# Performance work log

Hardware: AMD Instinct MI355X
Metric: run time of the kernel (lower is better)

The kernel has to match this reference:

```python
import jax, jax.numpy as jnp
import numpy as np

DIM = 4096
N_HEADS = 32
N_KV_HEADS = 8
HEAD_DIM = 128
EPS = 1e-6
B, S = 1, 2048


def setup_inputs() -> dict:
    key = jax.random.key(0)
    ks = jax.random.split(key, 8)
    x = jax.random.normal(ks[0], (B, S, DIM), dtype=jnp.float32)
    # Standard RoPE cos/sin table, broadcast to (B, S, HEAD_DIM)
    inv_freq = 1.0 / (10000.0 ** (np.arange(0, HEAD_DIM, 2, dtype=np.float32) / HEAD_DIM))
    t = np.arange(S, dtype=np.float32)
    freqs = np.outer(t, inv_freq)  # (S, HEAD_DIM/2)
    emb = np.concatenate([freqs, freqs], axis=-1)  # (S, HEAD_DIM)
    cos = jnp.broadcast_to(jnp.cos(emb)[None], (B, S, HEAD_DIM))
    sin = jnp.broadcast_to(jnp.sin(emb)[None], (B, S, HEAD_DIM))
    std = 0.02
    wq = jax.random.normal(ks[1], (N_HEADS * HEAD_DIM, DIM), dtype=jnp.float32) * std
    wk = jax.random.normal(ks[2], (N_KV_HEADS * HEAD_DIM, DIM), dtype=jnp.float32) * std
    wv = jax.random.normal(ks[3], (N_KV_HEADS * HEAD_DIM, DIM), dtype=jnp.float32) * std
    wo = jax.random.normal(ks[4], (DIM, N_HEADS * HEAD_DIM), dtype=jnp.float32) * std
    q_norm_w = jnp.ones((HEAD_DIM,), dtype=jnp.float32) + 0.1 * jax.random.normal(ks[5], (HEAD_DIM,), dtype=jnp.float32)
    k_norm_w = jnp.ones((HEAD_DIM,), dtype=jnp.float32) + 0.1 * jax.random.normal(ks[6], (HEAD_DIM,), dtype=jnp.float32)
    return {"x": x, "cos": cos, "sin": sin, "wq": wq, "wk": wk, "wv": wv,
            "wo": wo, "q_norm_w": q_norm_w, "k_norm_w": k_norm_w}


def _rmsnorm(x, w):
    var = jnp.mean(jnp.square(x), axis=-1, keepdims=True)
    return x * jax.lax.rsqrt(var + EPS) * w


def _rotate_half(x):
    h = x.shape[-1] // 2
    return jnp.concatenate([-x[..., h:], x[..., :h]], axis=-1)


def reference(x, cos, sin, wq, wk, wv, wo, q_norm_w, k_norm_w):
    bs, seqlen, _ = x.shape
    # QKV projections (Linear with weight of shape (out, in), no bias)
    xq = (x @ wq.T).reshape(bs, seqlen, N_HEADS, HEAD_DIM)
    xk = (x @ wk.T).reshape(bs, seqlen, N_KV_HEADS, HEAD_DIM)
    xv = (x @ wv.T).reshape(bs, seqlen, N_KV_HEADS, HEAD_DIM)
    # QK RMSNorm (after projection, before RoPE)
    xq = _rmsnorm(xq, q_norm_w)
    xk = _rmsnorm(xk, k_norm_w)
    # RoPE: cos/sin (B, S, D) -> broadcast over head axis
    c = cos[:, :, None, :]
    s = sin[:, :, None, :]
    xq = xq * c + _rotate_half(xq) * s
    xk = xk * c + _rotate_half(xk) * s
    # GQA: repeat kv heads
    n_rep = N_HEADS // N_KV_HEADS
    xk = jnp.repeat(xk, n_rep, axis=2)
    xv = jnp.repeat(xv, n_rep, axis=2)
    # (B, H, S, D)
    q = xq.transpose(0, 2, 1, 3)
    k = xk.transpose(0, 2, 1, 3)
    v = xv.transpose(0, 2, 1, 3)
    scale = HEAD_DIM ** -0.5
    scores = jnp.einsum('bhqd,bhkd->bhqk', q, k) * scale
    causal = jnp.tril(jnp.ones((seqlen, seqlen), dtype=bool))
    scores = jnp.where(causal, scores, jnp.finfo(scores.dtype).min)
    probs = jax.nn.softmax(scores, axis=-1)
    out = jnp.einsum('bhqk,bhkd->bhqd', probs, v)
    out = out.transpose(0, 2, 1, 3).reshape(bs, seqlen, N_HEADS * HEAD_DIM)
    return out @ wo.T
```

## Files before the change

kernel.cpp:

```cpp
#include <hip/hip_runtime.h>


#define S_LEN 2048
#define DIM 4096
#define NH 32
#define NKV 8
#define HD 128
#define SCALE 0.08838834764831845f

typedef __attribute__((ext_vector_type(8))) short short8;
typedef __attribute__((ext_vector_type(4))) float f32x4;

__device__ __forceinline__ float bf2f(unsigned short u) {
  union { unsigned i; float f; } c; c.i = ((unsigned)u) << 16; return c.f;
}
__device__ __forceinline__ unsigned short f2bf(float f) {
  union { float f; unsigned u; } c; c.f = f;
  return (unsigned short)((c.u + 0x7fffu + ((c.u >> 16) & 1u)) >> 16);
}
__device__ __forceinline__ void cvt8(const float* __restrict__ g,
                                     unsigned short* __restrict__ d) {
  const float4 a = *(const float4*)g;
  const float4 b = *(const float4*)(g + 4);
  short8 p;
  p[0] = (short)f2bf(a.x); p[1] = (short)f2bf(a.y);
  p[2] = (short)f2bf(a.z); p[3] = (short)f2bf(a.w);
  p[4] = (short)f2bf(b.x); p[5] = (short)f2bf(b.y);
  p[6] = (short)f2bf(b.z); p[7] = (short)f2bf(b.w);
  *(short8*)d = p;
}
__device__ __forceinline__ void storeC(float* p, float v) { *p = v; }
__device__ __forceinline__ void storeC(unsigned short* p, float v) { *p = f2bf(v); }

#define G_X   1048576u
#define G_WQ  2097152u
#define G_WK   524288u
#define G_WV   524288u
#define G_QKV (G_WQ + G_WK + G_WV)

__global__ __launch_bounds__(256)
void cvt_all(const float* __restrict__ x,  const float* __restrict__ wq,
             const float* __restrict__ wk, const float* __restrict__ wv,
             const float* __restrict__ wo,
             unsigned short* __restrict__ xb,
             unsigned short* __restrict__ wqkvb,
             unsigned short* __restrict__ wob) {
  const size_t g = (size_t)blockIdx.x * 256 + threadIdx.x;
  if (g < G_X) {
    cvt8(x + g * 8, xb + g * 8);
  } else if (g < G_X + G_QKV) {
    const size_t o = g - G_X;
    const float* s = (o < G_WQ) ? wq + o * 8
                   : (o < G_WQ + G_WK) ? wk + (o - G_WQ) * 8
                                       : wv + (o - G_WQ - G_WK) * 8;
    cvt8(s, wqkvb + o * 8);
  } else {
    const size_t o = g - (G_X + G_QKV);
    cvt8(wo + o * 8, wob + o * 8);
  }
}

template <int QKV, typename TC>
__global__ __launch_bounds__(256)
void gemm16(const unsigned short* __restrict__ A,
            const unsigned short* __restrict__ B,
            TC* __restrict__ C0,
            unsigned short* __restrict__ Ck,
            unsigned short* __restrict__ Cv, int K) {
  __shared__ unsigned short lsA[128 * 64];
  __shared__ unsigned short lsB[128 * 64];

  const int t    = threadIdx.x;
  const int lane = t & 63;
  const int w    = t >> 6;
  const int m0   = blockIdx.y * 128;
  const int n0   = blockIdx.x * 128;

  f32x4 acc[4][4];
#pragma unroll
  for (int a = 0; a < 4; ++a)
#pragma unroll
    for (int b = 0; b < 4; ++b)
#pragma unroll
      for (int e = 0; e < 4; ++e) acc[a][b][e] = 0.f;

  const int l15  = lane & 15;
  const int qd   = lane >> 4;
  const int wr   = w >> 1, wc = w & 1;
  const int sr8  = lane >> 3;
  const int skg  = (lane & 7) ^ sr8;
  const int l7   = l15 & 7;

  const int nkb = K >> 6;
  for (int kb = 0; kb < nkb; ++kb) {
    const int k0 = kb << 6;
#pragma unroll
    for (int c = 0; c < 4; ++c) {
      const int chunk = c * 4 + w;
      const int row   = chunk * 8 + sr8;
      const unsigned short* ga = A + (size_t)(m0 + row) * K + k0 + skg * 8;
      const unsigned short* gb = B + (size_t)(n0 + row) * K + k0 + skg * 8;
      __builtin_amdgcn_global_load_lds(
          (const __attribute__((address_space(1))) void*)ga,
          (__attribute__((address_space(3))) void*)(lsA + chunk * 512), 16, 0, 0);
      __builtin_amdgcn_global_load_lds(
          (const __attribute__((address_space(1))) void*)gb,
          (__attribute__((address_space(3))) void*)(lsB + chunk * 512), 16, 0, 0);
    }
    asm volatile("s_waitcnt vmcnt(0)" ::: "memory");
    __syncthreads();

#pragma unroll
    for (int half = 0; half < 2; ++half) {
      const int kg = (half * 4 + qd) ^ l7;
      short8 af[4], bf[4];
#pragma unroll
      for (int mi = 0; mi < 4; ++mi)
        af[mi] = *(const short8*)(lsA + (wr * 64 + mi * 16 + l15) * 64 + kg * 8);
#pragma unroll
      for (int ni = 0; ni < 4; ++ni)
        bf[ni] = *(const short8*)(lsB + (wc * 64 + ni * 16 + l15) * 64 + kg * 8);
#pragma unroll
      for (int mi = 0; mi < 4; ++mi)
#pragma unroll
        for (int ni = 0; ni < 4; ++ni)
          acc[mi][ni] = __builtin_amdgcn_mfma_f32_16x16x32_bf16(
              af[mi], bf[ni], acc[mi][ni], 0, 0, 0);
    }
    __syncthreads();
  }

#pragma unroll
  for (int mi = 0; mi < 4; ++mi)
#pragma unroll
    for (int i = 0; i < 4; ++i) {
      const int grow = m0 + wr * 64 + mi * 16 + qd * 4 + i;
#pragma unroll
      for (int ni = 0; ni < 4; ++ni) {
        const int gcol = n0 + wc * 64 + ni * 16 + l15;
        if (QKV) {
          if (n0 < 4096)
            storeC((unsigned short*)C0 + (size_t)grow * 4096 + gcol,
                   acc[mi][ni][i]);
          else if (n0 < 5120)
            Ck[(size_t)grow * 1024 + (gcol - 4096)] = f2bf(acc[mi][ni][i]);
          else
            Cv[(size_t)(gcol - 5120) * S_LEN + grow] = f2bf(acc[mi][ni][i]);
        } else {
          storeC(C0 + (size_t)grow * 4096 + gcol, acc[mi][ni][i]);
        }
      }
    }
}

__global__ __launch_bounds__(128)
void norm_rope(unsigned short* __restrict__ qb, unsigned short* __restrict__ kb,
               const float* __restrict__ cosb, const float* __restrict__ sinb,
               const float* __restrict__ qw, const float* __restrict__ kw) {
  const int hIdx = blockIdx.x;
  const int s    = blockIdx.y;
  const int d    = threadIdx.x;

  unsigned short* p; const float* wt;
  if (hIdx < NH) { p = qb + (size_t)s * (NH * HD) + hIdx * HD + d; wt = qw; }
  else           { p = kb + (size_t)s * (NKV * HD) + (hIdx - NH) * HD + d; wt = kw; }

  const float v = bf2f(*p);
  float ss = v * v;
  for (int off = 32; off; off >>= 1) ss += __shfl_down(ss, off);
  __shared__ float red[2];
  __shared__ float xs[128];
  if ((d & 63) == 0) red[d >> 6] = ss;
  __syncthreads();
  const float tot = red[0] + red[1];
  const float r   = rsqrtf(tot * (1.f / 128.f) + 1e-6f);
  const float xn  = v * r * wt[d];
  xs[d] = xn;
  __syncthreads();
  const float rot = (d < 64) ? -xs[d + 64] : xs[d - 64];
  float o = xn * cosb[s * HD + d] + rot * sinb[s * HD + d];
  if (hIdx < NH) o *= SCALE;
  *p = f2bf(o);
}

#define PSTR 72

__global__ __launch_bounds__(256)
void attn_mfma(const unsigned short* __restrict__ qB,
               const unsigned short* __restrict__ kB,
               const unsigned short* __restrict__ vT,
               unsigned short* __restrict__ oB) {
  __shared__ unsigned short ks[64 * 128];
  __shared__ unsigned short vt[128 * 64];
  __shared__ unsigned short Ps[4 * 16 * PSTR];

  const int t    = threadIdx.x;
  const int lane = t & 63;
  const int w    = t >> 6;
  const int qt   = (gridDim.x - 1) - blockIdx.x;
  const int h    = blockIdx.y;
  const int kvh  = h >> 2;
  const int l15  = lane & 15;
  const int qd   = lane >> 4;
  const int l7   = l15 & 7;

  const int kr16 = lane >> 4;
  const int vr8  = lane >> 3;
  const int vkg  = (lane & 7) ^ (vr8 & 7);

  short8 qf[4];
  {
    const unsigned short* qp =
        qB + (size_t)(qt * 64 + w * 16 + l15) * (NH * HD) + h * HD + qd * 8;
#pragma unroll
    for (int s = 0; s < 4; ++s) qf[s] = *(const short8*)(qp + s * 32);
  }

  f32x4 O[8];
#pragma unroll
  for (int nt = 0; nt < 8; ++nt)
#pragma unroll
    for (int e = 0; e < 4; ++e) O[nt][e] = 0.f;
  float l_i[4] = {0.f, 0.f, 0.f, 0.f};

  unsigned short* Pw = Ps + w * (16 * PSTR);

  for (int kt = 0; kt <= qt; ++kt) {
#pragma unroll
    for (int c = 0; c < 4; ++c) {
      const int chunk = w * 4 + c;
      const int key = chunk * 4 + kr16;
      const int dg  = (lane & 15) ^ (key & 15);
      const unsigned short* gk = kB + (size_t)(kt * 64 + key) * (NKV * HD) +
                                 kvh * HD + dg * 8;
      __builtin_amdgcn_global_load_lds(
          (const __attribute__((address_space(1))) void*)gk,
          (__attribute__((address_space(3))) void*)(ks + chunk * 512), 16, 0, 0);
      const int dv = chunk * 8 + vr8;
      const unsigned short* gv = vT + (size_t)(kvh * HD + dv) * S_LEN +
                                 kt * 64 + vkg * 8;
      __builtin_amdgcn_global_load_lds(
          (const __attribute__((address_space(1))) void*)gv,
          (__attribute__((address_space(3))) void*)(vt + chunk * 512), 16, 0, 0);
    }
    asm volatile("s_waitcnt vmcnt(0)" ::: "memory");
    __syncthreads();

    f32x4 S[4];
#pragma unroll
    for (int ct = 0; ct < 4; ++ct) {
#pragma unroll
      for (int e = 0; e < 4; ++e) S[ct][e] = 0.f;
#pragma unroll
      for (int s = 0; s < 4; ++s) {
        const int kg = (s * 4 + qd) ^ l15;
        const short8 kf =
            *(const short8*)(ks + (ct * 16 + l15) * 128 + kg * 8);
        S[ct] = __builtin_amdgcn_mfma_f32_16x16x32_bf16(qf[s], kf, S[ct], 0, 0, 0);
      }
    }

    if (kt == qt) {
#pragma unroll
      for (int ct = 0; ct < 4; ++ct)
#pragma unroll
        for (int i = 0; i < 4; ++i) {
          const int rloc = w * 16 + qd * 4 + i;
          const int cloc = ct * 16 + l15;
          if (cloc > rloc) S[ct][i] = -1e30f;
        }
    }

#pragma unroll
    for (int ct = 0; ct < 4; ++ct)
#pragma unroll
      for (int i = 0; i < 4; ++i) {
        const float e = __expf(S[ct][i]);
        l_i[i] += e;
        Pw[(qd * 4 + i) * PSTR + ct * 16 + l15] = f2bf(e);
      }

    {
      const short8 pf0 = *(const short8*)(Pw + l15 * PSTR + qd * 8);
      const short8 pf1 = *(const short8*)(Pw + l15 * PSTR + 32 + qd * 8);
#pragma unroll
      for (int nt = 0; nt < 8; ++nt) {
        const int kg0 = qd ^ l7;
        const int kg1 = (4 + qd) ^ l7;
        const short8 vf0 =
            *(const short8*)(vt + (nt * 16 + l15) * 64 + kg0 * 8);
        O[nt] = __builtin_amdgcn_mfma_f32_16x16x32_bf16(pf0, vf0, O[nt], 0, 0, 0);
        const short8 vf1 =
            *(const short8*)(vt + (nt * 16 + l15) * 64 + kg1 * 8);
        O[nt] = __builtin_amdgcn_mfma_f32_16x16x32_bf16(pf1, vf1, O[nt], 0, 0, 0);
      }
    }
    __syncthreads();
  }

  float linv[4];
#pragma unroll
  for (int i = 0; i < 4; ++i) {
    float s = l_i[i];
#pragma unroll
    for (int off = 1; off < 16; off <<= 1) s += __shfl_xor(s, off);
    linv[i] = 1.f / s;
  }
#pragma unroll
  for (int nt = 0; nt < 8; ++nt)
#pragma unroll
    for (int i = 0; i < 4; ++i) {
      const size_t row = (size_t)(qt * 64 + w * 16 + qd * 4 + i);
      oB[row * (NH * HD) + h * HD + nt * 16 + l15] = f2bf(O[nt][i] * linv[i]);
    }
}

extern "C" void kernel_launch(void* const* d_in, const int* in_sizes, int n_in,
                              void* d_out, int out_size, void* d_ws, size_t ws_size,
                              hipStream_t stream) {
  const float* x    = (const float*)d_in[0];
  const float* cosb = (const float*)d_in[1];
  const float* sinb = (const float*)d_in[2];
  const float* wq   = (const float*)d_in[3];
  const float* wk   = (const float*)d_in[4];
  const float* wv   = (const float*)d_in[5];
  const float* wo   = (const float*)d_in[6];
  const float* qnw  = (const float*)d_in[7];
  const float* knw  = (const float*)d_in[8];

  unsigned short* q     = (unsigned short*)d_ws;
  unsigned short* k     = q + (size_t)S_LEN * DIM;
  unsigned short* vT    = k + (size_t)S_LEN * NKV * HD;
  unsigned short* att   = vT + (size_t)NKV * HD * S_LEN;
  unsigned short* xb    = att + (size_t)S_LEN * DIM;
  unsigned short* wqkvb = xb + (size_t)S_LEN * DIM;
  unsigned short* wob   = wqkvb + (size_t)6144 * DIM;

  cvt_all<<<dim3(24576), dim3(256), 0, stream>>>(x, wq, wk, wv, wo, xb, wqkvb,
                                                 wob);
  gemm16<1, unsigned short>
      <<<dim3(48, 16), dim3(256), 0, stream>>>(xb, wqkvb, q, k, vT, DIM);
  norm_rope<<<dim3(NH + NKV, S_LEN), dim3(128), 0, stream>>>(q, k, cosb, sinb,
                                                             qnw, knw);
  attn_mfma<<<dim3(S_LEN / 64, NH), dim3(256), 0, stream>>>(q, k, vT, att);
  gemm16<0, float>
      <<<dim3(32, 16), dim3(256), 0, stream>>>(att, wob, (float*)d_out,
                                               nullptr, nullptr, DIM);
}
```

Baseline: 572.9 us.

## Replace 128x128 GEMM with 256x256 double-buffered pipelined GEMM using 8 waves

Replaces the single-buffered 128x128 tile GEMM with a 256x256 tile kernel of 512 threads. Half-tiles of A and B are staged into a 128KB double-buffered LDS region while MFMAs run on the other half, with barriers and s_setprio around the math. The aim is to hide global-load latency and raise data reuse per byte loaded. The catch is that the grid shrinks to 192 and 128 blocks, which is below one block per CU on a 256-CU part, and each block has one-block-per-CU LDS occupancy.

```diff
diff --git a/kernel.cpp b/kernel.cpp
--- a/kernel.cpp
+++ b/kernel.cpp
@@ -7,6 +7,7 @@
 #define NKV 8
 #define HD 128
 #define SCALE 0.08838834764831845f
+#define NKT 64
 
 typedef __attribute__((ext_vector_type(8))) short short8;
 typedef __attribute__((ext_vector_type(4))) float f32x4;
@@ -60,94 +61,144 @@
   }
 }
 
+
+#define STAGE(XB, G0, HH, KT, LOFF)                                           \
+  {                                                                            \
+    _Pragma("unroll")                                                          \
+    for (int j = 0; j < 2; ++j) {                                              \
+      const int chunk = (w << 1) + j;                                          \
+      const unsigned short* ga = (XB) +                                        \
+          (size_t)((G0) + (HH) * 128 + chunk * 8 + r8) * 4096 +                \
+          ((KT) << 6) + gsw;                                                   \
+      __builtin_amdgcn_global_load_lds(                                        \
+          (const __attribute__((address_space(1))) void*)ga,                   \
+          (__attribute__((address_space(3))) void*)(ls + (LOFF) +              \
+                                                    (HH) * 8192 + chunk * 512),\
+          16, 0, 0);                                                           \
+    }                                                                          \
+  }
+
+#define LDA(mq)                                                                \
+  _Pragma("unroll") for (int mi = 0; mi < 4; ++mi)                             \
+  _Pragma("unroll") for (int kc = 0; kc < 2; ++kc)                             \
+    af[mi][kc] = *(const short8*)(ls + aoff +                                  \
+        ((mq) * 128 + wr * 64 + mi * 16 + l15) * 64 +                          \
+        (((kc << 2) + qd) ^ l7) * 8);
+
+#define LDB(nq)                                                                \
+  _Pragma("unroll") for (int ni = 0; ni < 2; ++ni)                             \
+  _Pragma("unroll") for (int kc = 0; kc < 2; ++kc)                             \
+    bfr[nq][ni][kc] = *(const short8*)(ls + boff +                             \
+        ((nq) * 128 + wc * 32 + ni * 16 + l15) * 64 +                          \
+        (((kc << 2) + qd) ^ l7) * 8);
+
+#define MM(mq, nq)                                                             \
+  __builtin_amdgcn_s_setprio(1);                                               \
+  _Pragma("unroll") for (int mi = 0; mi < 4; ++mi)                             \
+  _Pragma("unroll") for (int ni = 0; ni < 2; ++ni)                             \
+  _Pragma("unroll") for (int kc = 0; kc < 2; ++kc)                             \
+    acc[(mq) * 4 + mi][(nq) * 2 + ni] =                                        \
+        __builtin_amdgcn_mfma_f32_16x16x32_bf16(                               \
+            af[mi][kc], bfr[nq][ni][kc], acc[(mq) * 4 + mi][(nq) * 2 + ni],    \
+            0, 0, 0);                                                          \
+  __builtin_amdgcn_s_setprio(0);
+
 template <int QKV, typename TC>
-__global__ __launch_bounds__(256)
-void gemm16(const unsigned short* __restrict__ A,
-            const unsigned short* __restrict__ B,
-            TC* __restrict__ C0,
-            unsigned short* __restrict__ Ck,
-            unsigned short* __restrict__ Cv, int K) {
-  __shared__ unsigned short lsA[128 * 64];
-  __shared__ unsigned short lsB[128 * 64];
+__global__ __launch_bounds__(512)
+void gemm256(const unsigned short* __restrict__ A,
+             const unsigned short* __restrict__ B,
+             TC* __restrict__ C0,
+             unsigned short* __restrict__ Ck,
+             unsigned short* __restrict__ Cv) {
+  __shared__ unsigned short ls[65536];
 
   const int t    = threadIdx.x;
   const int lane = t & 63;
   const int w    = t >> 6;
-  const int m0   = blockIdx.y * 128;
-  const int n0   = blockIdx.x * 128;
-
-  f32x4 acc[4][4];
-#pragma unroll
-  for (int a = 0; a < 4; ++a)
-#pragma unroll
-    for (int b = 0; b < 4; ++b)
-#pragma unroll
-      for (int e = 0; e < 4; ++e) acc[a][b][e] = 0.f;
-
+  const int wr   = w >> 2;
+  const int wc   = w & 3;
+  const int m0   = blockIdx.y * 256;
+  const int n0   = blockIdx.x * 256;
   const int l15  = lane & 15;
   const int qd   = lane >> 4;
-  const int wr   = w >> 1, wc = w & 1;
-  const int sr8  = lane >> 3;
-  const int skg  = (lane & 7) ^ sr8;
   const int l7   = l15 & 7;
-
-  const int nkb = K >> 6;
-  for (int kb = 0; kb < nkb; ++kb) {
-    const int k0 = kb << 6;
-#pragma unroll
-    for (int c = 0; c < 4; ++c) {
-      const int chunk = c * 4 + w;
-      const int row   = chunk * 8 + sr8;
-      const unsigned short* ga = A + (size_t)(m0 + row) * K + k0 + skg * 8;
-      const unsigned short* gb = B + (size_t)(n0 + row) * K + k0 + skg * 8;
-      __builtin_amdgcn_global_load_lds(
-          (const __attribute__((address_space(1))) void*)ga,
-          (__attribute__((address_space(3))) void*)(lsA + chunk * 512), 16, 0, 0);
-      __builtin_amdgcn_global_load_lds(
-          (const __attribute__((address_space(1))) void*)gb,
-          (__attribute__((address_space(3))) void*)(lsB + chunk * 512), 16, 0, 0);
-    }
-    asm volatile("s_waitcnt vmcnt(0)" ::: "memory");
-    __syncthreads();
-
-#pragma unroll
-    for (int half = 0; half < 2; ++half) {
-      const int kg = (half * 4 + qd) ^ l7;
-      short8 af[4], bf[4];
-#pragma unroll
-      for (int mi = 0; mi < 4; ++mi)
-        af[mi] = *(const short8*)(lsA + (wr * 64 + mi * 16 + l15) * 64 + kg * 8);
-#pragma unroll
-      for (int ni = 0; ni < 4; ++ni)
-        bf[ni] = *(const short8*)(lsB + (wc * 64 + ni * 16 + l15) * 64 + kg * 8);
-#pragma unroll
-      for (int mi = 0; mi < 4; ++mi)
-#pragma unroll
-        for (int ni = 0; ni < 4; ++ni)
-          acc[mi][ni] = __builtin_amdgcn_mfma_f32_16x16x32_bf16(
-              af[mi], bf[ni], acc[mi][ni], 0, 0, 0);
-    }
-    __syncthreads();
-  }
-
-#pragma unroll
-  for (int mi = 0; mi < 4; ++mi)
+  const int r8   = lane >> 3;
+  const int gsw  = ((lane & 7) ^ r8) * 8;
+
+  f32x4 acc[8][4];
+#pragma unroll
+  for (int a = 0; a < 8; ++a)
+#pragma unroll
+    for (int b = 0; b < 4; ++b)
+#pragma unroll
+      for (int e = 0; e < 4; ++e) acc[a][b][e] = 0.f;
+
+  short8 af[4][2];
+  short8 bfr[2][2][2];
+
+  STAGE(A, m0, 0, 0, 0);
+  STAGE(B, n0, 1, 0, 16384);
+  STAGE(A, m0, 1, 0, 0);
+  STAGE(B, n0, 0, 0, 16384);
+  STAGE(A, m0, 0, 1, 32768);
+  STAGE(B, n0, 1, 1, 49152);
+  asm volatile("s_waitcnt vmcnt(4)" ::: "memory");
+  __builtin_amdgcn_s_barrier();
+
+#pragma unroll 2
+  for (int kt = 0; kt < NKT; ++kt) {
+    const int p    = kt & 1;
+    const int base = p << 15;
+    const int ob   = base ^ 32768;
+    const int aoff = base;
+    const int boff = base + 16384;
+    const int kn1  = (kt + 1 < NKT) ? kt + 1 : NKT - 1;
+    const int kn2  = (kt + 2 < NKT) ? kt + 2 : NKT - 1;
+
+    LDA(0);
+    LDB(0);
+    STAGE(A, m0, 1, kn1, ob);
+    __builtin_amdgcn_s_barrier();
+    MM(0, 0);
+    __builtin_amdgcn_s_barrier();
+
+    LDB(1);
+    STAGE(B, n0, 0, kn1, ob + 16384);
+    __builtin_amdgcn_s_barrier();
+    MM(0, 1);
+    __builtin_amdgcn_s_barrier();
+
+    LDA(1);
+    STAGE(A, m0, 0, kn2, base);
+    __builtin_amdgcn_s_barrier();
+    MM(1, 1);
+    __builtin_amdgcn_s_barrier();
+
+    STAGE(B, n0, 1, kn2, base + 16384);
+    __builtin_amdgcn_s_barrier();
+    MM(1, 0);
+    asm volatile("s_waitcnt vmcnt(4)" ::: "memory");
+    __builtin_amdgcn_s_barrier();
+  }
+
+#pragma unroll
+  for (int fm = 0; fm < 8; ++fm)
 #pragma unroll
     for (int i = 0; i < 4; ++i) {
-      const int grow = m0 + wr * 64 + mi * 16 + qd * 4 + i;
-#pragma unroll
-      for (int ni = 0; ni < 4; ++ni) {
-        const int gcol = n0 + wc * 64 + ni * 16 + l15;
+      const int grow = m0 + (fm >> 2) * 128 + wr * 64 + (fm & 3) * 16 + qd * 4 + i;
+#pragma unroll
+      for (int fn = 0; fn < 4; ++fn) {
+        const int gcol = n0 + (fn >> 1) * 128 + wc * 32 + (fn & 1) * 16 + l15;
+        const float v  = acc[fm][fn][i];
         if (QKV) {
           if (n0 < 4096)
-            storeC((unsigned short*)C0 + (size_t)grow * 4096 + gcol,
-                   acc[mi][ni][i]);
+            storeC((unsigned short*)C0 + (size_t)grow * 4096 + gcol, v);
           else if (n0 < 5120)
-            Ck[(size_t)grow * 1024 + (gcol - 4096)] = f2bf(acc[mi][ni][i]);
+            Ck[(size_t)grow * 1024 + (gcol - 4096)] = f2bf(v);
           else
-            Cv[(size_t)(gcol - 5120) * S_LEN + grow] = f2bf(acc[mi][ni][i]);
+            Cv[(size_t)(gcol - 5120) * S_LEN + grow] = f2bf(v);
         } else {
-          storeC(C0 + (size_t)grow * 4096 + gcol, acc[mi][ni][i]);
+          storeC(C0 + (size_t)grow * 4096 + gcol, v);
         }
       }
     }
@@ -338,12 +389,12 @@
 
   cvt_all<<<dim3(24576), dim3(256), 0, stream>>>(x, wq, wk, wv, wo, xb, wqkvb,
                                                  wob);
-  gemm16<1, unsigned short>
-      <<<dim3(48, 16), dim3(256), 0, stream>>>(xb, wqkvb, q, k, vT, DIM);
+  gemm256<1, unsigned short>
+      <<<dim3(24, 8), dim3(512), 0, stream>>>(xb, wqkvb, q, k, vT);
   norm_rope<<<dim3(NH + NKV, S_LEN), dim3(128), 0, stream>>>(q, k, cosb, sinb,
                                                              qnw, knw);
   attn_mfma<<<dim3(S_LEN / 64, NH), dim3(256), 0, stream>>>(q, k, vT, att);
-  gemm16<0, float>
-      <<<dim3(32, 16), dim3(256), 0, stream>>>(att, wob, (float*)d_out,
-                                               nullptr, nullptr, DIM);
-}
+  gemm256<0, float>
+      <<<dim3(16, 8), dim3(512), 0, stream>>>(att, wob, (float*)d_out,
+                                              nullptr, nullptr);
+}
```

New measurement: 589.7 us. +2.9%, slower.

## Double attention query tile to 128 rows per block and streamline norm_rope

Applied to the files above, without the earlier changes.

The attention kernel now handles 128 query rows per block, with each wave owning two 16-row fragments. Each K/V tile loaded into LDS is therefore reused by twice as many MFMAs, which halves K/V global traffic per query. On the diagonal tile, waves whose rows are fully masked skip their work, and query tiles are ordered in reverse for half the heads to balance load across blocks. norm_rope is rewritten so one wave handles a whole head, using wave shuffles with no LDS or barriers, and each block processes 8 heads. The cost is higher register pressure from doubled accumulators and fewer, larger attention blocks (16x32 grid).

```diff
diff --git a/kernel.cpp b/kernel.cpp
--- a/kernel.cpp
+++ b/kernel.cpp
@@ -153,34 +153,35 @@
     }
 }
 
-__global__ __launch_bounds__(128)
+__global__ __launch_bounds__(512)
 void norm_rope(unsigned short* __restrict__ qb, unsigned short* __restrict__ kb,
                const float* __restrict__ cosb, const float* __restrict__ sinb,
                const float* __restrict__ qw, const float* __restrict__ kw) {
-  const int hIdx = blockIdx.x;
-  const int s    = blockIdx.y;
-  const int d    = threadIdx.x;
+  const int s    = blockIdx.x;
+  const int w    = threadIdx.x >> 6;
+  const int l    = threadIdx.x & 63;
+  const int hh   = blockIdx.y * 8 + w;
 
   unsigned short* p; const float* wt;
-  if (hIdx < NH) { p = qb + (size_t)s * (NH * HD) + hIdx * HD + d; wt = qw; }
-  else           { p = kb + (size_t)s * (NKV * HD) + (hIdx - NH) * HD + d; wt = kw; }
-
-  const float v = bf2f(*p);
-  float ss = v * v;
-  for (int off = 32; off; off >>= 1) ss += __shfl_down(ss, off);
-  __shared__ float red[2];
-  __shared__ float xs[128];
-  if ((d & 63) == 0) red[d >> 6] = ss;
-  __syncthreads();
-  const float tot = red[0] + red[1];
-  const float r   = rsqrtf(tot * (1.f / 128.f) + 1e-6f);
-  const float xn  = v * r * wt[d];
-  xs[d] = xn;
-  __syncthreads();
-  const float rot = (d < 64) ? -xs[d + 64] : xs[d - 64];
-  float o = xn * cosb[s * HD + d] + rot * sinb[s * HD + d];
-  if (hIdx < NH) o *= SCALE;
-  *p = f2bf(o);
+  if (hh < NH) { p = qb + (size_t)s * (NH * HD) + hh * HD; wt = qw; }
+  else         { p = kb + (size_t)s * (NKV * HD) + (hh - NH) * HD; wt = kw; }
+
+  const float v0 = bf2f(p[l]);
+  const float v1 = bf2f(p[l + 64]);
+  float ss = v0 * v0 + v1 * v1;
+#pragma unroll
+  for (int off = 32; off; off >>= 1) ss += __shfl_xor(ss, off);
+  const float r = rsqrtf(ss * (1.f / 128.f) + 1e-6f);
+
+  const float xn0 = v0 * r * wt[l];
+  const float xn1 = v1 * r * wt[l + 64];
+  const float c0 = cosb[s * HD + l],      s0 = sinb[s * HD + l];
+  const float c1 = cosb[s * HD + l + 64], s1 = sinb[s * HD + l + 64];
+  float o0 = xn0 * c0 - xn1 * s0;
+  float o1 = xn1 * c1 + xn0 * s1;
+  if (hh < NH) { o0 *= SCALE; o1 *= SCALE; }
+  p[l]      = f2bf(o0);
+  p[l + 64] = f2bf(o1);
 }
 
 #define PSTR 72
@@ -192,13 +193,14 @@
                unsigned short* __restrict__ oB) {
   __shared__ unsigned short ks[64 * 128];
   __shared__ unsigned short vt[128 * 64];
-  __shared__ unsigned short Ps[4 * 16 * PSTR];
+  __shared__ unsigned short Ps[4 * 32 * PSTR];
 
   const int t    = threadIdx.x;
   const int lane = t & 63;
   const int w    = t >> 6;
-  const int qt   = (gridDim.x - 1) - blockIdx.x;
   const int h    = blockIdx.y;
+  const int qt   = (h & 16) ? (15 - blockIdx.x) : blockIdx.x;
+  const int q0   = qt * 128;
   const int kvh  = h >> 2;
   const int l15  = lane & 15;
   const int qd   = lane >> 4;
@@ -208,24 +210,28 @@
   const int vr8  = lane >> 3;
   const int vkg  = (lane & 7) ^ (vr8 & 7);
 
-  short8 qf[4];
-  {
+  short8 qf[2][4];
+#pragma unroll
+  for (int f = 0; f < 2; ++f) {
     const unsigned short* qp =
-        qB + (size_t)(qt * 64 + w * 16 + l15) * (NH * HD) + h * HD + qd * 8;
-#pragma unroll
-    for (int s = 0; s < 4; ++s) qf[s] = *(const short8*)(qp + s * 32);
+        qB + (size_t)(q0 + w * 32 + f * 16 + l15) * (NH * HD) + h * HD + qd * 8;
+#pragma unroll
+    for (int s = 0; s < 4; ++s) qf[f][s] = *(const short8*)(qp + s * 32);
   }
 
-  f32x4 O[8];
-#pragma unroll
-  for (int nt = 0; nt < 8; ++nt)
-#pragma unroll
-    for (int e = 0; e < 4; ++e) O[nt][e] = 0.f;
-  float l_i[4] = {0.f, 0.f, 0.f, 0.f};
-
-  unsigned short* Pw = Ps + w * (16 * PSTR);
-
-  for (int kt = 0; kt <= qt; ++kt) {
+  f32x4 O[2][8];
+#pragma unroll
+  for (int f = 0; f < 2; ++f)
+#pragma unroll
+    for (int nt = 0; nt < 8; ++nt)
+#pragma unroll
+      for (int e = 0; e < 4; ++e) O[f][nt][e] = 0.f;
+  float l_i[2][4] = {{0.f, 0.f, 0.f, 0.f}, {0.f, 0.f, 0.f, 0.f}};
+
+  unsigned short* Pw = Ps + w * (32 * PSTR);
+
+  const int nkt = 2 * qt + 2;
+  for (int kt = 0; kt < nkt; ++kt) {
 #pragma unroll
     for (int c = 0; c < 4; ++c) {
       const int chunk = w * 4 + c;
@@ -246,73 +252,99 @@
     asm volatile("s_waitcnt vmcnt(0)" ::: "memory");
     __syncthreads();
 
-    f32x4 S[4];
-#pragma unroll
-    for (int ct = 0; ct < 4; ++ct) {
-#pragma unroll
-      for (int e = 0; e < 4; ++e) S[ct][e] = 0.f;
-#pragma unroll
-      for (int s = 0; s < 4; ++s) {
-        const int kg = (s * 4 + qd) ^ l15;
-        const short8 kf =
-            *(const short8*)(ks + (ct * 16 + l15) * 128 + kg * 8);
-        S[ct] = __builtin_amdgcn_mfma_f32_16x16x32_bf16(qf[s], kf, S[ct], 0, 0, 0);
-      }
-    }
-
-    if (kt == qt) {
-#pragma unroll
-      for (int ct = 0; ct < 4; ++ct)
-#pragma unroll
-        for (int i = 0; i < 4; ++i) {
-          const int rloc = w * 16 + qd * 4 + i;
-          const int cloc = ct * 16 + l15;
-          if (cloc > rloc) S[ct][i] = -1e30f;
+    const int dk = kt - 2 * qt;
+    const bool active = (dk <= 0) || (w >= 2);
+    if (active) {
+      f32x4 S[2][4];
+#pragma unroll
+      for (int ct = 0; ct < 4; ++ct) {
+#pragma unroll
+        for (int e = 0; e < 4; ++e) { S[0][ct][e] = 0.f; S[1][ct][e] = 0.f; }
+#pragma unroll
+        for (int s = 0; s < 4; ++s) {
+          const int kg = (s * 4 + qd) ^ l15;
+          const short8 kf =
+              *(const short8*)(ks + (ct * 16 + l15) * 128 + kg * 8);
+          S[0][ct] = __builtin_amdgcn_mfma_f32_16x16x32_bf16(qf[0][s], kf,
+                                                             S[0][ct], 0, 0, 0);
+          S[1][ct] = __builtin_amdgcn_mfma_f32_16x16x32_bf16(qf[1][s], kf,
+                                                             S[1][ct], 0, 0, 0);
         }
-    }
-
-#pragma unroll
-    for (int ct = 0; ct < 4; ++ct)
-#pragma unroll
-      for (int i = 0; i < 4; ++i) {
-        const float e = __expf(S[ct][i]);
-        l_i[i] += e;
-        Pw[(qd * 4 + i) * PSTR + ct * 16 + l15] = f2bf(e);
-      }
-
-    {
-      const short8 pf0 = *(const short8*)(Pw + l15 * PSTR + qd * 8);
-      const short8 pf1 = *(const short8*)(Pw + l15 * PSTR + 32 + qd * 8);
-#pragma unroll
-      for (int nt = 0; nt < 8; ++nt) {
+      }
+
+      if (dk >= 0) {
+#pragma unroll
+        for (int f = 0; f < 2; ++f)
+#pragma unroll
+          for (int ct = 0; ct < 4; ++ct)
+#pragma unroll
+            for (int i = 0; i < 4; ++i) {
+              const int krel = dk * 64 + ct * 16 + l15;
+              const int rrel = w * 32 + f * 16 + qd * 4 + i;
+              if (krel > rrel) S[f][ct][i] = -1e30f;
+            }
+      }
+
+#pragma unroll
+      for (int f = 0; f < 2; ++f)
+#pragma unroll
+        for (int ct = 0; ct < 4; ++ct)
+#pragma unroll
+          for (int i = 0; i < 4; ++i) {
+            const float e = __expf(S[f][ct][i]);
+            l_i[f][i] += e;
+            Pw[(f * 16 + qd * 4 + i) * PSTR + ct * 16 + l15] = f2bf(e);
+          }
+
+      {
+        short8 pf[2][2];
+#pragma unroll
+        for (int f = 0; f < 2; ++f) {
+          pf[f][0] = *(const short8*)(Pw + (f * 16 + l15) * PSTR + qd * 8);
+          pf[f][1] = *(const short8*)(Pw + (f * 16 + l15) * PSTR + 32 + qd * 8);
+        }
         const int kg0 = qd ^ l7;
         const int kg1 = (4 + qd) ^ l7;
-        const short8 vf0 =
-            *(const short8*)(vt + (nt * 16 + l15) * 64 + kg0 * 8);
-        O[nt] = __builtin_amdgcn_mfma_f32_16x16x32_bf16(pf0, vf0, O[nt], 0, 0, 0);
-        const short8 vf1 =
-            *(const short8*)(vt + (nt * 16 + l15) * 64 + kg1 * 8);
-        O[nt] = __builtin_amdgcn_mfma_f32_16x16x32_bf16(pf1, vf1, O[nt], 0, 0, 0);
+#pragma unroll
+        for (int nt = 0; nt < 8; ++nt) {
+          const short8 vf0 =
+              *(const short8*)(vt + (nt * 16 + l15) * 64 + kg0 * 8);
+          const short8 vf1 =
+              *(const short8*)(vt + (nt * 16 + l15) * 64 + kg1 * 8);
+          O[0][nt] = __builtin_amdgcn_mfma_f32_16x16x32_bf16(pf[0][0], vf0,
+                                                             O[0][nt], 0, 0, 0);
+          O[1][nt] = __builtin_amdgcn_mfma_f32_16x16x32_bf16(pf[1][0], vf0,
+                                                             O[1][nt], 0, 0, 0);
+          O[0][nt] = __builtin_amdgcn_mfma_f32_16x16x32_bf16(pf[0][1], vf1,
+                                                             O[0][nt], 0, 0, 0);
+          O[1][nt] = __builtin_amdgcn_mfma_f32_16x16x32_bf16(pf[1][1], vf1,
+                                                             O[1][nt], 0, 0, 0);
+        }
       }
     }
     __syncthreads();
   }
 
-  float linv[4];
-#pragma unroll
-  for (int i = 0; i < 4; ++i) {
-    float s = l_i[i];
-#pragma unroll
-    for (int off = 1; off < 16; off <<= 1) s += __shfl_xor(s, off);
-    linv[i] = 1.f / s;
-  }
-#pragma unroll
-  for (int nt = 0; nt < 8; ++nt)
+  float linv[2][4];
+#pragma unroll
+  for (int f = 0; f < 2; ++f)
 #pragma unroll
     for (int i = 0; i < 4; ++i) {
-      const size_t row = (size_t)(qt * 64 + w * 16 + qd * 4 + i);
-      oB[row * (NH * HD) + h * HD + nt * 16 + l15] = f2bf(O[nt][i] * linv[i]);
-    }
+      float s = l_i[f][i];
+#pragma unroll
+      for (int off = 1; off < 16; off <<= 1) s += __shfl_xor(s, off);
+      linv[f][i] = 1.f / s;
+    }
+#pragma unroll
+  for (int f = 0; f < 2; ++f)
+#pragma unroll
+    for (int nt = 0; nt < 8; ++nt)
+#pragma unroll
+      for (int i = 0; i < 4; ++i) {
+        const size_t row = (size_t)(q0 + w * 32 + f * 16 + qd * 4 + i);
+        oB[row * (NH * HD) + h * HD + nt * 16 + l15] =
+            f2bf(O[f][nt][i] * linv[f][i]);
+      }
 }
 
 extern "C" void kernel_launch(void* const* d_in, const int* in_sizes, int n_in,
@@ -340,9 +372,9 @@
                                                  wob);
   gemm16<1, unsigned short>
       <<<dim3(48, 16), dim3(256), 0, stream>>>(xb, wqkvb, q, k, vT, DIM);
-  norm_rope<<<dim3(NH + NKV, S_LEN), dim3(128), 0, stream>>>(q, k, cosb, sinb,
-                                                             qnw, knw);
-  attn_mfma<<<dim3(S_LEN / 64, NH), dim3(256), 0, stream>>>(q, k, vT, att);
+  norm_rope<<<dim3(S_LEN, 5), dim3(512), 0, stream>>>(q, k, cosb, sinb,
+                                                      qnw, knw);
+  attn_mfma<<<dim3(S_LEN / 128, NH), dim3(256), 0, stream>>>(q, k, vT, att);
   gemm16<0, float>
       <<<dim3(32, 16), dim3(256), 0, stream>>>(att, wob, (float*)d_out,
                                                nullptr, nullptr, DIM);
```

New measurement: 533.0 us. 7.0% less time.
